# Kernel optimization log

Measured on AMD Instinct MI355X. Metric: run time of the kernel, lower is better.

## Reference

```python
import jax, jax.numpy as jnp
import numpy as np

B, S, D, H = 4, 1024, 2048, 16
DH = D // H  # 128
THETA = 10000.0


def setup_inputs() -> dict:
    key = jax.random.key(0)
    k1, k2, k3 = jax.random.split(key, 3)
    std_qkv = np.sqrt(2.0 / (D + 3 * D)).astype(np.float32)
    std_out = np.sqrt(2.0 / (D + D)).astype(np.float32)
    x = jax.random.normal(k1, (B, S, D), jnp.float32)
    w_qkv = jax.random.normal(k2, (D, 3 * D), jnp.float32) * std_qkv
    w_out = jax.random.normal(k3, (D, D), jnp.float32) * std_out
    # matrix-based RoPE table: [max_seq, d_head//2, 2, 2]
    freqs = jnp.arange(S, dtype=jnp.float32)[:, None] / THETA ** (
        2.0 * jnp.arange(DH // 2, dtype=jnp.float32) / DH)[None, :]
    eye = jnp.array([[1.0, 0.0], [0.0, 1.0]], jnp.float32)
    rot = jnp.array([[0.0, -1.0], [1.0, 0.0]], jnp.float32)
    rope_matrix = (jnp.cos(freqs)[:, :, None, None] * eye
                   + jnp.sin(freqs)[:, :, None, None] * rot)
    token_positions = jnp.arange(S, dtype=jnp.int32)
    return {"x": x, "w_qkv": w_qkv, "w_out": w_out,
            "rope_matrix": rope_matrix, "token_positions": token_positions}


def _apply_rope(t, pe):
    # t: [B, H, S, DH]; pe: [S, DH//2, 2, 2] (gathered by token_positions)
    tr = t.reshape(*t.shape[:-1], DH // 2, 2)  # interleaved (even, odd) pairs
    out = jnp.einsum('bhski,skoi->bhsko', tr, pe)
    return out.reshape(t.shape)


def reference(x, w_qkv, w_out, rope_matrix, token_positions):
    qkv = jnp.einsum('bsd,df->bsf', x, w_qkv)          # [B,S,3D]
    q, k, v = jnp.split(qkv, 3, axis=-1)
    to_heads = lambda t: t.reshape(B, S, H, DH).transpose(0, 2, 1, 3)
    q, k, v = to_heads(q), to_heads(k), to_heads(v)    # [B,H,S,DH]
    pe = rope_matrix[token_positions]                  # [S, DH//2, 2, 2]
    q = _apply_rope(q, pe)
    k = _apply_rope(k, pe)
    scores = jnp.einsum('bhqd,bhkd->bhqk', q, k) / np.float32(np.sqrt(DH))
    causal = jnp.tril(jnp.ones((S, S), dtype=bool))
    scores = jnp.where(causal, scores, -jnp.inf)
    attn = jax.nn.softmax(scores, axis=-1)
    ctx = jnp.einsum('bhqk,bhkd->bhqd', attn, v)       # [B,H,S,DH]
    ctx = ctx.transpose(0, 2, 1, 3).reshape(B, S, D)
    return jnp.einsum('bsd,df->bsf', ctx, w_out)
```

## Files before the change

kernel.cpp:

```cpp
#include <hip/hip_runtime.h>
#include <hip/hip_bf16.h>
#include <math.h>

#define Bn 4
#define Sn 1024
#define Dn 2048
#define Hn 16
#define DHn 128
#define BS (Bn * Sn)
#define QKVC (3 * Dn)

typedef __attribute__((ext_vector_type(8))) short short8;
typedef __attribute__((ext_vector_type(4))) float float4v;

__device__ inline unsigned short f2bf(float x) {
  union { float f; unsigned int u; } v; v.f = x;
  unsigned int r = v.u + 0x7fffu + ((v.u >> 16) & 1u);
  return (unsigned short)(r >> 16);
}
__device__ inline float bf2f(unsigned short b) {
  union { unsigned int u; float f; } v; v.u = ((unsigned int)b) << 16;
  return v.f;
}

__device__ __forceinline__ void gload16(const unsigned short* g, unsigned short* l) {
  __builtin_amdgcn_global_load_lds(
      (const __attribute__((address_space(1))) unsigned int*)g,
      (__attribute__((address_space(3))) unsigned int*)l, 16, 0, 0);
}

__device__ void tc_body(const float* __restrict__ w, unsigned short* __restrict__ wT,
                        int K, int N, int bx, int by, int tid,
                        unsigned short (*t)[72]) {
  const int c0 = bx * 64;
  const int r0 = by * 64;
  const int r = tid >> 2;
  const int cb = (tid & 3) * 16;
#pragma unroll
  for (int it = 0; it < 4; ++it) {
    float4 v = *reinterpret_cast<const float4*>(&w[(long)(r0 + r) * N + c0 + cb + 4 * it]);
    t[r][cb + 4 * it + 0] = f2bf(v.x);
    t[r][cb + 4 * it + 1] = f2bf(v.y);
    t[r][cb + 4 * it + 2] = f2bf(v.z);
    t[r][cb + 4 * it + 3] = f2bf(v.w);
  }
  __syncthreads();
  unsigned short o[16];
#pragma unroll
  for (int e = 0; e < 16; ++e) o[e] = t[cb + e][r];
  unsigned short* dst = &wT[(long)(c0 + r) * K + r0 + cb];
  *reinterpret_cast<short8*>(dst) = *reinterpret_cast<short8*>(&o[0]);
  *reinterpret_cast<short8*>(dst + 8) = *reinterpret_cast<short8*>(&o[8]);
}

__global__ __launch_bounds__(256) void prep_all(
    const float* __restrict__ x, const float* __restrict__ w_qkv,
    const float* __restrict__ w_out, unsigned short* __restrict__ x16,
    unsigned short* __restrict__ wqkvT, unsigned short* __restrict__ woutT) {
  __shared__ unsigned short t[64][72];
  const int bid = blockIdx.x;
  const int tid = threadIdx.x;
  if (bid < 4096) {
    const int id = bid * 256 + tid;
    const float4* p = reinterpret_cast<const float4*>(x) + 2 * (size_t)id;
    float4 a = p[0], b = p[1];
    short8 o;
    o[0] = (short)f2bf(a.x); o[1] = (short)f2bf(a.y);
    o[2] = (short)f2bf(a.z); o[3] = (short)f2bf(a.w);
    o[4] = (short)f2bf(b.x); o[5] = (short)f2bf(b.y);
    o[6] = (short)f2bf(b.z); o[7] = (short)f2bf(b.w);
    *reinterpret_cast<short8*>(x16 + 8 * (size_t)id) = o;
  } else if (bid < 7168) {
    const int lb = bid - 4096;
    tc_body(w_qkv, wqkvT, Dn, QKVC, lb % 96, lb / 96, tid, t);
  } else {
    const int lb = bid - 7168;
    tc_body(w_out, woutT, Dn, Dn, lb % 32, lb / 32, tid, t);
  }
}

#define AB8(buf, h) ((buf) * 16384 + (h) * 8192)
#define BB8(buf) (32768 + (buf) * 8192)

#define VMW(n)                                                                 \
  asm volatile("s_waitcnt vmcnt(" #n ")" ::: "memory");                        \
  __builtin_amdgcn_sched_barrier(0);

#define PHASE(BUF, MIH, STAGE_STMT, WAIT_STMT)                                 \
  {                                                                            \
    __builtin_amdgcn_sched_barrier(0);                                         \
    short8 afr[2][2];                                                          \
    _Pragma("unroll") for (int mi2 = 0; mi2 < 2; ++mi2) {                      \
      const int mrow = wr * 64 + ((MIH) * 2 + mi2) * 16;                       \
      const int hh = mrow >> 7;                                                \
      const int rl = (mrow & 127) + c;                                         \
      _Pragma("unroll") for (int ks = 0; ks < 2; ++ks)                         \
        afr[mi2][ks] = *(const short8*)(lds + AB8(BUF, 0) + hh * 8192 +        \
            rl * 64 + (((ks * 4 + g) ^ cg7) << 3));                            \
    }                                                                          \
    if ((MIH) == 0) {                                                          \
      _Pragma("unroll") for (int ni = 0; ni < 4; ++ni)                         \
        _Pragma("unroll") for (int ks = 0; ks < 2; ++ks)                       \
          bfr[ni][ks] = *(const short8*)(lds + BB8(BUF) +                      \
              (wc * 64 + ni * 16 + c) * 64 + (((ks * 4 + g) ^ cg7) << 3));     \
    }                                                                          \
    STAGE_STMT;                                                                \
    __builtin_amdgcn_sched_barrier(0);                                         \
    __builtin_amdgcn_s_barrier();                                              \
    asm volatile("s_waitcnt lgkmcnt(0)" ::: "memory");                         \
    __builtin_amdgcn_sched_barrier(0);                                         \
    __builtin_amdgcn_s_setprio(1);                                             \
    _Pragma("unroll") for (int mi2 = 0; mi2 < 2; ++mi2)                        \
      _Pragma("unroll") for (int ni = 0; ni < 4; ++ni)                         \
        _Pragma("unroll") for (int ks = 0; ks < 2; ++ks)                       \
          acc[(MIH) * 2 + mi2][ni] = __builtin_amdgcn_mfma_f32_16x16x32_bf16(  \
              afr[mi2][ks], bfr[ni][ks], acc[(MIH) * 2 + mi2][ni], 0, 0, 0);   \
    __builtin_amdgcn_s_setprio(0);                                             \
    WAIT_STMT                                                                  \
    __builtin_amdgcn_s_barrier();                                              \
  }

#define GEMM_MAIN_LOOP(A_, BT_, K_)                                            \
  STAGE(A_ + (long)m0 * K_, AB8(0, 0));                                        \
  STAGE(A_ + (long)(m0 + 128) * K_, AB8(0, 1));                                \
  STAGE(BT_ + (long)n0 * K_, BB8(0));                                          \
  STAGE(BT_ + (long)n0 * K_ + 64, BB8(1));                                     \
  VMW(2)                                                                       \
  __builtin_amdgcn_s_barrier();                                                \
  for (int it2 = 0; it2 < nt / 2 - 1; ++it2) {                                 \
    const long T1 = (long)(2 * it2 + 1) * 64;                                  \
    const long T2 = (long)(2 * it2 + 2) * 64;                                  \
    const long T3 = (long)(2 * it2 + 3) * 64;                                  \
    PHASE(0, 0, STAGE(A_ + (long)m0 * K_ + T1, AB8(1, 0)), )                   \
    PHASE(0, 1,                                                                \
          { STAGE(A_ + (long)(m0 + 128) * K_ + T1, AB8(1, 1));                 \
            STAGE(BT_ + (long)n0 * K_ + T2, BB8(0)); }, VMW(2))                \
    PHASE(1, 0, STAGE(A_ + (long)m0 * K_ + T2, AB8(0, 0)), )                   \
    PHASE(1, 1,                                                                \
          { STAGE(A_ + (long)(m0 + 128) * K_ + T2, AB8(0, 1));                 \
            STAGE(BT_ + (long)n0 * K_ + T3, BB8(1)); }, VMW(2))                \
  }                                                                            \
  {                                                                            \
    const long TL = (long)(nt - 1) * 64;                                       \
    PHASE(0, 0, STAGE(A_ + (long)m0 * K_ + TL, AB8(1, 0)), )                   \
    PHASE(0, 1, STAGE(A_ + (long)(m0 + 128) * K_ + TL, AB8(1, 1)), VMW(0))     \
    PHASE(1, 0, {}, )                                                          \
    PHASE(1, 1, {}, )                                                          \
  }

__global__ __launch_bounds__(512, 2) void gemm_qkv(
    const unsigned short* __restrict__ A, const unsigned short* __restrict__ BT,
    const float* __restrict__ rope, const int* __restrict__ tpos,
    unsigned short* __restrict__ qR, unsigned short* __restrict__ kR,
    unsigned short* __restrict__ vT, int K) {
  __shared__ unsigned short lds[49152];
  const int tid = threadIdx.x;
  const int wid = tid >> 6, lane = tid & 63;
  const int c = lane & 15, g = lane >> 4;
  const int wr = wid >> 1, wc = wid & 1;
  const int cg7 = c & 7;

  const int nwg = gridDim.x * gridDim.y;
  const int bid = blockIdx.y * gridDim.x + blockIdx.x;
  const int swz = (bid & 7) * (nwg >> 3) + (bid >> 3);
  const int m0 = (swz % gridDim.x) * 256, n0 = (swz / gridDim.x) * 128;

  const int nt = K >> 6;

  float4v acc[4][4];
#pragma unroll
  for (int i = 0; i < 4; ++i)
#pragma unroll
    for (int j = 0; j < 4; ++j) acc[i][j] = (float4v){0.f, 0.f, 0.f, 0.f};
  short8 bfr[4][2];

  auto STAGE = [&](const unsigned short* gbase, int sbase) {
#pragma unroll
    for (int j = 0; j < 2; ++j) {
      const int ch = j * 512 + tid;
      const int r = ch >> 3;
      const int wo = (ch & 7) ^ (r & 7);
      gload16(gbase + (long)r * K + wo * 8, lds + sbase + j * 4096 + wid * 512);
    }
  };

  GEMM_MAIN_LOOP(A, BT, K)

  const int type = n0 >> 11;
  const int h = (n0 & 2047) >> 7;
  const long bh = (long)((m0 >> 10) * Hn + h);
  const int s0 = m0 & 1023;

  if (type == 2) {
#pragma unroll
    for (int mi = 0; mi < 4; ++mi)
#pragma unroll
      for (int ni = 0; ni < 4; ++ni)
#pragma unroll
        for (int j = 0; j < 4; ++j) {
          const int mm = wr * 64 + mi * 16 + g * 4 + j;
          const int nn = wc * 64 + ni * 16 + c;
          lds[nn * 264 + mm] = f2bf(acc[mi][ni][j]);
        }
    __syncthreads();
    unsigned short* dst = vT + bh * (long)DHn * Sn + s0;
#pragma unroll
    for (int it = 0; it < 8; ++it) {
      const int cid = it * 512 + tid;
      const int d = cid >> 5;
      const int sl = (cid & 31) * 8;
      short8 v = *reinterpret_cast<const short8*>(lds + d * 264 + sl);
      *reinterpret_cast<short8*>(dst + (long)d * Sn + sl) = v;
    }
  } else {
#pragma unroll
    for (int mi = 0; mi < 4; ++mi)
#pragma unroll
      for (int ni = 0; ni < 4; ++ni)
#pragma unroll
        for (int j = 0; j < 4; ++j) {
          const int mm = wr * 64 + mi * 16 + g * 4 + j;
          const int nn = wc * 64 + ni * 16 + c;
          lds[mm * 136 + nn] = f2bf(acc[mi][ni][j]);
        }
    __syncthreads();
    unsigned short* dst = (type == 0 ? qR : kR) + (bh * Sn + s0) * DHn;
    const float qsc = (type == 0) ? 0.1275174213f : 1.0f;
#pragma unroll
    for (int it = 0; it < 8; ++it) {
      const int cid = it * 512 + tid;
      const int r = cid >> 4;
      const int colc = (cid & 15) * 8;
      union { short8 v; unsigned short u[8]; } iw, ow;
      iw.v = *reinterpret_cast<const short8*>(lds + r * 136 + colc);
      const int pos = tpos[s0 + r];
      const float4* pe = reinterpret_cast<const float4*>(rope) +
                         (long)pos * 64 + (colc >> 1);
#pragma unroll
      for (int p = 0; p < 4; ++p) {
        const float4 m2 = pe[p];
        const float xx = bf2f(iw.u[2 * p]), yy = bf2f(iw.u[2 * p + 1]);
        ow.u[2 * p]     = f2bf((m2.x * xx + m2.y * yy) * qsc);
        ow.u[2 * p + 1] = f2bf((m2.z * xx + m2.w * yy) * qsc);
      }
      *reinterpret_cast<short8*>(dst + (long)r * DHn + colc) = ow.v;
    }
  }
}

__global__ __launch_bounds__(512, 2) void gemm_out(
    const unsigned short* __restrict__ A, const unsigned short* __restrict__ BT,
    float* __restrict__ Cout, int N, int K) {
  __shared__ unsigned short lds[49152];
  const int tid = threadIdx.x;
  const int wid = tid >> 6, lane = tid & 63;
  const int c = lane & 15, g = lane >> 4;
  const int wr = wid >> 1, wc = wid & 1;
  const int cg7 = c & 7;

  const int nwg = gridDim.x * gridDim.y;
  const int bid = blockIdx.y * gridDim.x + blockIdx.x;
  const int swz = (bid & 7) * (nwg >> 3) + (bid >> 3);
  const int m0 = (swz % gridDim.x) * 256, n0 = (swz / gridDim.x) * 128;

  const int nt = K >> 6;

  float4v acc[4][4];
#pragma unroll
  for (int i = 0; i < 4; ++i)
#pragma unroll
    for (int j = 0; j < 4; ++j) acc[i][j] = (float4v){0.f, 0.f, 0.f, 0.f};
  short8 bfr[4][2];

  auto STAGE = [&](const unsigned short* gbase, int sbase) {
#pragma unroll
    for (int j = 0; j < 2; ++j) {
      const int ch = j * 512 + tid;
      const int r = ch >> 3;
      const int wo = (ch & 7) ^ (r & 7);
      gload16(gbase + (long)r * K + wo * 8, lds + sbase + j * 4096 + wid * 512);
    }
  };

  GEMM_MAIN_LOOP(A, BT, K)

#pragma unroll
  for (int mi = 0; mi < 4; ++mi)
#pragma unroll
    for (int ni = 0; ni < 4; ++ni)
#pragma unroll
      for (int j = 0; j < 4; ++j) {
        const int m = m0 + wr * 64 + mi * 16 + g * 4 + j;
        const int n = n0 + wc * 64 + ni * 16 + c;
        Cout[(long)m * N + n] = acc[mi][ni][j];
      }
}
#undef PHASE
#undef GEMM_MAIN_LOOP

__global__ __launch_bounds__(256, 2) void attn_mfma(
    const unsigned short* __restrict__ qR, const unsigned short* __restrict__ kR,
    const unsigned short* __restrict__ vTd, unsigned short* __restrict__ ctx) {
  __shared__ unsigned short lds[32768];
  __shared__ unsigned short Ps[4][16][72];
  const int qp = gridDim.x - 1 - blockIdx.x;
  const int h = blockIdx.y, b = blockIdx.z;
  const int tid = threadIdx.x, wid = tid >> 6, lane = tid & 63;
  const int c = lane & 15, g = lane >> 4, cg7 = c & 7;
  const long bh = (long)(b * Hn + h);
  const unsigned short* kbase = kR + bh * Sn * DHn;
  const unsigned short* vbase = vTd + bh * DHn * Sn;

  short8 qf[2][4];
#pragma unroll
  for (int sub = 0; sub < 2; ++sub) {
    const unsigned short* qrow =
        qR + (bh * Sn + qp * 128 + sub * 64 + wid * 16 + c) * DHn;
#pragma unroll
    for (int kc = 0; kc < 4; ++kc)
      qf[sub][kc] = *reinterpret_cast<const short8*>(qrow + kc * 32 + g * 8);
  }

  auto STAGE = [&](int kt, int buf) {
#pragma unroll
    for (int j = 0; j < 4; ++j) {
      const int ch = j * 256 + tid;
      const int r = ch >> 4, wd = ch & 15;
      const int ws = (wd & 8) | ((wd & 7) ^ (r & 7));
      gload16(kbase + (long)kt * 8192 + r * 128 + ws * 8,
              lds + buf * 8192 + j * 2048 + wid * 512);
    }
#pragma unroll
    for (int j = 0; j < 4; ++j) {
      const int ch = j * 256 + tid;
      const int d = ch >> 3, sw = ch & 7;
      gload16(vbase + (long)d * Sn + kt * 64 + ((sw ^ (d & 7)) << 3),
              lds + 16384 + buf * 8192 + j * 2048 + wid * 512);
    }
  };

  float m[2] = {-INFINITY, -INFINITY}, lsum[2] = {0.f, 0.f};
  float4v otA[8], otB[8];
#pragma unroll
  for (int fd = 0; fd < 8; ++fd) {
    otA[fd] = (float4v){0.f, 0.f, 0.f, 0.f};
    otB[fd] = (float4v){0.f, 0.f, 0.f, 0.f};
  }

  const int ntt = 2 * qp + 2;
  STAGE(0, 0);
  __syncthreads();
  int cur = 0;

  for (int kt = 0; kt < ntt; ++kt) {
    if (kt + 1 < ntt) STAGE(kt + 1, cur ^ 1);

#pragma unroll
    for (int sub = 0; sub < 2; ++sub) {
      if (sub == 0 && kt == ntt - 1) continue;
      float4v* ot = (sub == 0) ? otA : otB;

      float4v scv[4];
#pragma unroll
      for (int f = 0; f < 4; ++f) scv[f] = (float4v){0.f, 0.f, 0.f, 0.f};
      __builtin_amdgcn_s_setprio(1);
#pragma unroll
      for (int f = 0; f < 4; ++f)
#pragma unroll
        for (int kc = 0; kc < 4; ++kc) {
          const int wp = kc * 4 + g;
          const int ws = (wp & 8) | ((wp & 7) ^ cg7);
          short8 kf = *reinterpret_cast<const short8*>(
              lds + cur * 8192 + (f * 16 + c) * 128 + ws * 8);
          scv[f] = __builtin_amdgcn_mfma_f32_16x16x32_bf16(kf, qf[sub][kc],
                                                           scv[f], 0, 0, 0);
        }
      __builtin_amdgcn_s_setprio(0);

      if (kt == 2 * qp + sub) {
        const int qloc = wid * 16 + c;
#pragma unroll
        for (int f = 0; f < 4; ++f)
#pragma unroll
          for (int j = 0; j < 4; ++j)
            if (f * 16 + g * 4 + j > qloc) scv[f][j] = -INFINITY;
      }

      float tmax = -INFINITY;
#pragma unroll
      for (int f = 0; f < 4; ++f)
#pragma unroll
        for (int j = 0; j < 4; ++j) tmax = fmaxf(tmax, scv[f][j]);
      tmax = fmaxf(tmax, __shfl_xor(tmax, 16));
      tmax = fmaxf(tmax, __shfl_xor(tmax, 32));

      float mnew, corr;
      if (__all(tmax <= m[sub] + 8.f)) {
        mnew = m[sub]; corr = 1.f;
      } else {
        mnew = fmaxf(m[sub], tmax);
        corr = exp2f(m[sub] - mnew);
#pragma unroll
        for (int fd = 0; fd < 8; ++fd) ot[fd] *= corr;
      }
      float psum = 0.f;
#pragma unroll
      for (int f = 0; f < 4; ++f)
#pragma unroll
        for (int j = 0; j < 4; ++j) {
          scv[f][j] = exp2f(scv[f][j] - mnew);
          psum += scv[f][j];
        }
      psum += __shfl_xor(psum, 16);
      psum += __shfl_xor(psum, 32);
      lsum[sub] = lsum[sub] * corr + psum;
      m[sub] = mnew;

#pragma unroll
      for (int f = 0; f < 4; ++f) {
        unsigned int lo = (unsigned)f2bf(scv[f][0]) | ((unsigned)f2bf(scv[f][1]) << 16);
        unsigned int hi = (unsigned)f2bf(scv[f][2]) | ((unsigned)f2bf(scv[f][3]) << 16);
        uint2 pk; pk.x = lo; pk.y = hi;
        *reinterpret_cast<uint2*>(&Ps[wid][c][f * 16 + g * 4]) = pk;
      }

      short8 pf0 = *reinterpret_cast<const short8*>(&Ps[wid][c][g * 8]);
      short8 pf1 = *reinterpret_cast<const short8*>(&Ps[wid][c][32 + g * 8]);
      __builtin_amdgcn_s_setprio(1);
#pragma unroll
      for (int fd = 0; fd < 8; ++fd) {
        short8 vf0 = *reinterpret_cast<const short8*>(
            lds + 16384 + cur * 8192 + (fd * 16 + c) * 64 + ((g ^ cg7) << 3));
        short8 vf1 = *reinterpret_cast<const short8*>(
            lds + 16384 + cur * 8192 + (fd * 16 + c) * 64 + (((g + 4) ^ cg7) << 3));
        ot[fd] = __builtin_amdgcn_mfma_f32_16x16x32_bf16(vf0, pf0, ot[fd], 0, 0, 0);
        ot[fd] = __builtin_amdgcn_mfma_f32_16x16x32_bf16(vf1, pf1, ot[fd], 0, 0, 0);
      }
      __builtin_amdgcn_s_setprio(0);
    }

    __syncthreads();
    cur ^= 1;
  }

#pragma unroll
  for (int sub = 0; sub < 2; ++sub) {
    const float4v* ot = (sub == 0) ? otA : otB;
    const float inv = 1.0f / lsum[sub];
    unsigned short* orow =
        ctx + (long)(b * Sn + qp * 128 + sub * 64 + wid * 16 + c) * Dn + h * DHn;
#pragma unroll
    for (int fd = 0; fd < 8; ++fd) {
      const int d = fd * 16 + g * 4;
      uint2 pk;
      pk.x = (unsigned)f2bf(ot[fd][0] * inv) | ((unsigned)f2bf(ot[fd][1] * inv) << 16);
      pk.y = (unsigned)f2bf(ot[fd][2] * inv) | ((unsigned)f2bf(ot[fd][3] * inv) << 16);
      *reinterpret_cast<uint2*>(orow + d) = pk;
    }
  }
}

extern "C" void kernel_launch(void* const* d_in, const int* in_sizes, int n_in,
                              void* d_out, int out_size, void* d_ws, size_t ws_size,
                              hipStream_t stream) {
  const float* x     = (const float*)d_in[0];
  const float* w_qkv = (const float*)d_in[1];
  const float* w_out = (const float*)d_in[2];
  const float* rope  = (const float*)d_in[3];
  const int*   tpos  = (const int*)d_in[4];
  float* out = (float*)d_out;

  unsigned short* x16    = (unsigned short*)d_ws;
  unsigned short* wqkvT  = x16 + (size_t)BS * Dn;
  unsigned short* woutT  = wqkvT + (size_t)Dn * QKVC;
  unsigned short* qR     = woutT + (size_t)Dn * Dn;
  unsigned short* kR     = qR + (size_t)BS * Dn;
  unsigned short* vT16   = kR + (size_t)BS * Dn;
  unsigned short* ctx16  = vT16 + (size_t)BS * Dn;

  prep_all<<<8192, 256, 0, stream>>>(x, w_qkv, w_out, x16, wqkvT, woutT);
  {
    dim3 grid(BS / 256, QKVC / 128);
    gemm_qkv<<<grid, 512, 0, stream>>>(x16, wqkvT, rope, tpos, qR, kR, vT16, Dn);
  }
  {
    dim3 grid(Sn / 128, Hn, Bn);
    attn_mfma<<<grid, 256, 0, stream>>>(qR, kR, vT16, ctx16);
  }
  {
    dim3 grid(BS / 256, Dn / 128);
    gemm_out<<<grid, 512, 0, stream>>>(ctx16, woutT, out, Dn, Dn);
  }
}
```

Before: 250.6 us.

## Switch QKV and output GEMMs to 128x128 tiles with simple double-buffered loop

Both projection GEMMs now use 128x128 output tiles on 256-thread blocks instead of 256x128 tiles on 512 threads. The hand-scheduled four-phase pipeline with explicit vmcnt waits and split barriers is replaced by a plain double-buffered loop with __syncthreads. This doubles the grid, shrinks LDS use per block, and simplifies scheduling, which may improve occupancy and tail behaviour. In exchange it loses the fine-grained overlap of loads and MFMA and reuses each A and B element less per tile.

```diff
diff --git a/kernel.cpp b/kernel.cpp
--- a/kernel.cpp
+++ b/kernel.cpp
@@ -79,81 +79,45 @@
   }
 }
 
-#define AB8(buf, h) ((buf) * 16384 + (h) * 8192)
-#define BB8(buf) (32768 + (buf) * 8192)
-
-#define VMW(n)                                                                 \
-  asm volatile("s_waitcnt vmcnt(" #n ")" ::: "memory");                        \
-  __builtin_amdgcn_sched_barrier(0);
-
-#define PHASE(BUF, MIH, STAGE_STMT, WAIT_STMT)                                 \
-  {                                                                            \
-    __builtin_amdgcn_sched_barrier(0);                                         \
-    short8 afr[2][2];                                                          \
-    _Pragma("unroll") for (int mi2 = 0; mi2 < 2; ++mi2) {                      \
-      const int mrow = wr * 64 + ((MIH) * 2 + mi2) * 16;                       \
-      const int hh = mrow >> 7;                                                \
-      const int rl = (mrow & 127) + c;                                         \
+#define ABUF(buf) ((buf) * 8192)
+#define BBUF(buf) (16384 + (buf) * 8192)
+
+#define GEMM128_LOOP(A_, BT_, K_)                                              \
+  STAGE(A_ + (long)m0 * K_, ABUF(0));                                          \
+  STAGE(BT_ + (long)n0 * K_, BBUF(0));                                         \
+  __syncthreads();                                                             \
+  for (int t = 0; t < nt; ++t) {                                               \
+    const int cb = t & 1;                                                      \
+    if (t + 1 < nt) {                                                          \
+      const long To = (long)(t + 1) * 64;                                      \
+      STAGE(A_ + (long)m0 * K_ + To, ABUF(cb ^ 1));                            \
+      STAGE(BT_ + (long)n0 * K_ + To, BBUF(cb ^ 1));                           \
+    }                                                                          \
+    short8 afr[4][2], bfr[4][2];                                               \
+    _Pragma("unroll") for (int mi = 0; mi < 4; ++mi)                           \
       _Pragma("unroll") for (int ks = 0; ks < 2; ++ks)                         \
-        afr[mi2][ks] = *(const short8*)(lds + AB8(BUF, 0) + hh * 8192 +        \
-            rl * 64 + (((ks * 4 + g) ^ cg7) << 3));                            \
-    }                                                                          \
-    if ((MIH) == 0) {                                                          \
+        afr[mi][ks] = *(const short8*)(lds + ABUF(cb) +                        \
+            (wr * 64 + mi * 16 + c) * 64 + (((ks * 4 + g) ^ cg7) << 3));       \
+    _Pragma("unroll") for (int ni = 0; ni < 4; ++ni)                           \
+      _Pragma("unroll") for (int ks = 0; ks < 2; ++ks)                         \
+        bfr[ni][ks] = *(const short8*)(lds + BBUF(cb) +                        \
+            (wc * 64 + ni * 16 + c) * 64 + (((ks * 4 + g) ^ cg7) << 3));       \
+    __builtin_amdgcn_s_setprio(1);                                             \
+    _Pragma("unroll") for (int mi = 0; mi < 4; ++mi)                           \
       _Pragma("unroll") for (int ni = 0; ni < 4; ++ni)                         \
         _Pragma("unroll") for (int ks = 0; ks < 2; ++ks)                       \
-          bfr[ni][ks] = *(const short8*)(lds + BB8(BUF) +                      \
-              (wc * 64 + ni * 16 + c) * 64 + (((ks * 4 + g) ^ cg7) << 3));     \
-    }                                                                          \
-    STAGE_STMT;                                                                \
-    __builtin_amdgcn_sched_barrier(0);                                         \
-    __builtin_amdgcn_s_barrier();                                              \
-    asm volatile("s_waitcnt lgkmcnt(0)" ::: "memory");                         \
-    __builtin_amdgcn_sched_barrier(0);                                         \
-    __builtin_amdgcn_s_setprio(1);                                             \
-    _Pragma("unroll") for (int mi2 = 0; mi2 < 2; ++mi2)                        \
-      _Pragma("unroll") for (int ni = 0; ni < 4; ++ni)                         \
-        _Pragma("unroll") for (int ks = 0; ks < 2; ++ks)                       \
-          acc[(MIH) * 2 + mi2][ni] = __builtin_amdgcn_mfma_f32_16x16x32_bf16(  \
-              afr[mi2][ks], bfr[ni][ks], acc[(MIH) * 2 + mi2][ni], 0, 0, 0);   \
+          acc[mi][ni] = __builtin_amdgcn_mfma_f32_16x16x32_bf16(               \
+              afr[mi][ks], bfr[ni][ks], acc[mi][ni], 0, 0, 0);                 \
     __builtin_amdgcn_s_setprio(0);                                             \
-    WAIT_STMT                                                                  \
-    __builtin_amdgcn_s_barrier();                                              \
-  }
-
-#define GEMM_MAIN_LOOP(A_, BT_, K_)                                            \
-  STAGE(A_ + (long)m0 * K_, AB8(0, 0));                                        \
-  STAGE(A_ + (long)(m0 + 128) * K_, AB8(0, 1));                                \
-  STAGE(BT_ + (long)n0 * K_, BB8(0));                                          \
-  STAGE(BT_ + (long)n0 * K_ + 64, BB8(1));                                     \
-  VMW(2)                                                                       \
-  __builtin_amdgcn_s_barrier();                                                \
-  for (int it2 = 0; it2 < nt / 2 - 1; ++it2) {                                 \
-    const long T1 = (long)(2 * it2 + 1) * 64;                                  \
-    const long T2 = (long)(2 * it2 + 2) * 64;                                  \
-    const long T3 = (long)(2 * it2 + 3) * 64;                                  \
-    PHASE(0, 0, STAGE(A_ + (long)m0 * K_ + T1, AB8(1, 0)), )                   \
-    PHASE(0, 1,                                                                \
-          { STAGE(A_ + (long)(m0 + 128) * K_ + T1, AB8(1, 1));                 \
-            STAGE(BT_ + (long)n0 * K_ + T2, BB8(0)); }, VMW(2))                \
-    PHASE(1, 0, STAGE(A_ + (long)m0 * K_ + T2, AB8(0, 0)), )                   \
-    PHASE(1, 1,                                                                \
-          { STAGE(A_ + (long)(m0 + 128) * K_ + T2, AB8(0, 1));                 \
-            STAGE(BT_ + (long)n0 * K_ + T3, BB8(1)); }, VMW(2))                \
-  }                                                                            \
-  {                                                                            \
-    const long TL = (long)(nt - 1) * 64;                                       \
-    PHASE(0, 0, STAGE(A_ + (long)m0 * K_ + TL, AB8(1, 0)), )                   \
-    PHASE(0, 1, STAGE(A_ + (long)(m0 + 128) * K_ + TL, AB8(1, 1)), VMW(0))     \
-    PHASE(1, 0, {}, )                                                          \
-    PHASE(1, 1, {}, )                                                          \
-  }
-
-__global__ __launch_bounds__(512, 2) void gemm_qkv(
+    __syncthreads();                                                           \
+  }
+
+__global__ __launch_bounds__(256, 2) void gemm_qkv(
     const unsigned short* __restrict__ A, const unsigned short* __restrict__ BT,
     const float* __restrict__ rope, const int* __restrict__ tpos,
     unsigned short* __restrict__ qR, unsigned short* __restrict__ kR,
     unsigned short* __restrict__ vT, int K) {
-  __shared__ unsigned short lds[49152];
+  __shared__ unsigned short lds[32768];
   const int tid = threadIdx.x;
   const int wid = tid >> 6, lane = tid & 63;
   const int c = lane & 15, g = lane >> 4;
@@ -163,7 +127,7 @@
   const int nwg = gridDim.x * gridDim.y;
   const int bid = blockIdx.y * gridDim.x + blockIdx.x;
   const int swz = (bid & 7) * (nwg >> 3) + (bid >> 3);
-  const int m0 = (swz % gridDim.x) * 256, n0 = (swz / gridDim.x) * 128;
+  const int m0 = (swz % gridDim.x) * 128, n0 = (swz / gridDim.x) * 128;
 
   const int nt = K >> 6;
 
@@ -172,19 +136,18 @@
   for (int i = 0; i < 4; ++i)
 #pragma unroll
     for (int j = 0; j < 4; ++j) acc[i][j] = (float4v){0.f, 0.f, 0.f, 0.f};
-  short8 bfr[4][2];
 
   auto STAGE = [&](const unsigned short* gbase, int sbase) {
 #pragma unroll
-    for (int j = 0; j < 2; ++j) {
-      const int ch = j * 512 + tid;
+    for (int j = 0; j < 4; ++j) {
+      const int ch = j * 256 + tid;
       const int r = ch >> 3;
       const int wo = (ch & 7) ^ (r & 7);
-      gload16(gbase + (long)r * K + wo * 8, lds + sbase + j * 4096 + wid * 512);
+      gload16(gbase + (long)r * K + wo * 8, lds + sbase + j * 2048 + wid * 512);
     }
   };
 
-  GEMM_MAIN_LOOP(A, BT, K)
+  GEMM128_LOOP(A, BT, K)
 
   const int type = n0 >> 11;
   const int h = (n0 & 2047) >> 7;
@@ -200,16 +163,16 @@
         for (int j = 0; j < 4; ++j) {
           const int mm = wr * 64 + mi * 16 + g * 4 + j;
           const int nn = wc * 64 + ni * 16 + c;
-          lds[nn * 264 + mm] = f2bf(acc[mi][ni][j]);
+          lds[nn * 136 + mm] = f2bf(acc[mi][ni][j]);
         }
     __syncthreads();
     unsigned short* dst = vT + bh * (long)DHn * Sn + s0;
 #pragma unroll
     for (int it = 0; it < 8; ++it) {
-      const int cid = it * 512 + tid;
-      const int d = cid >> 5;
-      const int sl = (cid & 31) * 8;
-      short8 v = *reinterpret_cast<const short8*>(lds + d * 264 + sl);
+      const int cid = it * 256 + tid;
+      const int d = cid >> 4;
+      const int sl = (cid & 15) * 8;
+      short8 v = *reinterpret_cast<const short8*>(lds + d * 136 + sl);
       *reinterpret_cast<short8*>(dst + (long)d * Sn + sl) = v;
     }
   } else {
@@ -228,7 +191,7 @@
     const float qsc = (type == 0) ? 0.1275174213f : 1.0f;
 #pragma unroll
     for (int it = 0; it < 8; ++it) {
-      const int cid = it * 512 + tid;
+      const int cid = it * 256 + tid;
       const int r = cid >> 4;
       const int colc = (cid & 15) * 8;
       union { short8 v; unsigned short u[8]; } iw, ow;
@@ -248,10 +211,10 @@
   }
 }
 
-__global__ __launch_bounds__(512, 2) void gemm_out(
+__global__ __launch_bounds__(256, 2) void gemm_out(
     const unsigned short* __restrict__ A, const unsigned short* __restrict__ BT,
     float* __restrict__ Cout, int N, int K) {
-  __shared__ unsigned short lds[49152];
+  __shared__ unsigned short lds[32768];
   const int tid = threadIdx.x;
   const int wid = tid >> 6, lane = tid & 63;
   const int c = lane & 15, g = lane >> 4;
@@ -261,7 +224,7 @@
   const int nwg = gridDim.x * gridDim.y;
   const int bid = blockIdx.y * gridDim.x + blockIdx.x;
   const int swz = (bid & 7) * (nwg >> 3) + (bid >> 3);
-  const int m0 = (swz % gridDim.x) * 256, n0 = (swz / gridDim.x) * 128;
+  const int m0 = (swz % gridDim.x) * 128, n0 = (swz / gridDim.x) * 128;
 
   const int nt = K >> 6;
 
@@ -270,19 +233,18 @@
   for (int i = 0; i < 4; ++i)
 #pragma unroll
     for (int j = 0; j < 4; ++j) acc[i][j] = (float4v){0.f, 0.f, 0.f, 0.f};
-  short8 bfr[4][2];
 
   auto STAGE = [&](const unsigned short* gbase, int sbase) {
 #pragma unroll
-    for (int j = 0; j < 2; ++j) {
-      const int ch = j * 512 + tid;
+    for (int j = 0; j < 4; ++j) {
+      const int ch = j * 256 + tid;
       const int r = ch >> 3;
       const int wo = (ch & 7) ^ (r & 7);
-      gload16(gbase + (long)r * K + wo * 8, lds + sbase + j * 4096 + wid * 512);
+      gload16(gbase + (long)r * K + wo * 8, lds + sbase + j * 2048 + wid * 512);
     }
   };
 
-  GEMM_MAIN_LOOP(A, BT, K)
+  GEMM128_LOOP(A, BT, K)
 
 #pragma unroll
   for (int mi = 0; mi < 4; ++mi)
@@ -295,8 +257,7 @@
         Cout[(long)m * N + n] = acc[mi][ni][j];
       }
 }
-#undef PHASE
-#undef GEMM_MAIN_LOOP
+#undef GEMM128_LOOP
 
 __global__ __launch_bounds__(256, 2) void attn_mfma(
     const unsigned short* __restrict__ qR, const unsigned short* __restrict__ kR,
@@ -480,15 +441,15 @@
 
   prep_all<<<8192, 256, 0, stream>>>(x, w_qkv, w_out, x16, wqkvT, woutT);
   {
-    dim3 grid(BS / 256, QKVC / 128);
-    gemm_qkv<<<grid, 512, 0, stream>>>(x16, wqkvT, rope, tpos, qR, kR, vT16, Dn);
+    dim3 grid(BS / 128, QKVC / 128);
+    gemm_qkv<<<grid, 256, 0, stream>>>(x16, wqkvT, rope, tpos, qR, kR, vT16, Dn);
   }
   {
     dim3 grid(Sn / 128, Hn, Bn);
     attn_mfma<<<grid, 256, 0, stream>>>(qR, kR, vT16, ctx16);
   }
   {
-    dim3 grid(BS / 256, Dn / 128);
-    gemm_out<<<grid, 512, 0, stream>>>(ctx16, woutT, out, Dn, Dn);
-  }
-}
+    dim3 grid(BS / 128, Dn / 128);
+    gemm_out<<<grid, 256, 0, stream>>>(ctx16, woutT, out, Dn, Dn);
+  }
+}
```

Result: faster. 242.9 us (-3.1%).
